# Kernel optimization log

Hardware: AMD Instinct MI355X
Metric: run time of the kernel (lower is better)

## Reference

```python
import jax, jax.numpy as jnp
import numpy as np

DIM = 2048
NUM_HEADS = 16
HEAD_DIM = DIM // NUM_HEADS  # 128
HIDDEN = HEAD_DIM * NUM_HEADS  # 2048


def setup_inputs() -> dict:
    key = jax.random.key(0)
    k1, k2, k3 = jax.random.split(key, 3)
    x = jax.random.normal(k1, (2, 4096, DIM), dtype=jnp.float32)
    # match torch init: gates.weight ~ N(0, dim**-0.5), output.weight ~ N(0, hidden**-0.5)
    Wg = jax.random.normal(k2, (NUM_HEADS + 3 * HIDDEN, DIM), dtype=jnp.float32) * DIM ** -0.5
    bg = jnp.zeros((NUM_HEADS + 3 * HIDDEN,), dtype=jnp.float32)
    Wo = jax.random.normal(k3, (DIM, HIDDEN), dtype=jnp.float32) * HIDDEN ** -0.5
    bo = jnp.zeros((DIM,), dtype=jnp.float32)
    return {"x": x, "Wg": Wg, "bg": bg, "Wo": Wo, "bo": bo}


def _combine(a, b):
    # linear recurrence c_t = f_t * c_{t-1} + u_t as an associative op
    fa, ua = a
    fb, ub = b
    return fa * fb, fb * ua + ub


def reference(x, Wg, bg, Wo, bo):
    # x: [B, T, dim]
    g = jnp.einsum('btd,gd->btg', x, Wg) + bg  # [B, T, H + 3*hidden]
    f = jax.nn.sigmoid(g[..., :NUM_HEADS])  # [B, T, H]
    i = jax.nn.sigmoid(g[..., NUM_HEADS:NUM_HEADS + HIDDEN])
    t = jnp.tanh(g[..., NUM_HEADS + HIDDEN:NUM_HEADS + 2 * HIDDEN])
    o = g[..., NUM_HEADS + 2 * HIDDEN:]
    f = jnp.repeat(f, HEAD_DIM, axis=-1)  # tied forget gate per head -> [B, T, hidden]
    update = i * t
    # scan over time axis (axis=1)
    _, c = jax.lax.associative_scan(_combine, (f, update), axis=1)
    h = o * jnp.tanh(c)
    return jnp.einsum('bth,dh->btd', h, Wo) + bo
```

## Files before the change

kernel.cpp:

```cpp
#include <hip/hip_runtime.h>
#include <hip/hip_bf16.h>

#define DIM 2048
#define NHEADS 16
#define HEAD_DIM 128
#define HIDDEN 2048
#define SEQ 4096
#define BATCH 2
#define BT (BATCH * SEQ)
#define NSEG 64
#define SEGLEN (SEQ / NSEG)
#define N_GATE (3 * HIDDEN)

typedef __bf16 bf16_t;
typedef __bf16 bf16x8 __attribute__((ext_vector_type(8)));
typedef __bf16 bf16x4_t __attribute__((ext_vector_type(4)));
typedef float f32x4 __attribute__((ext_vector_type(4)));

__device__ __forceinline__ void gload_lds16(const void* g, void* l) {
  __builtin_amdgcn_global_load_lds(
      (const __attribute__((address_space(1))) void*)g,
      (__attribute__((address_space(3))) void*)l, 16, 0, 0);
}

#define MEMFENCE asm volatile("" ::: "memory")
#define BAR do { MEMFENCE; __builtin_amdgcn_s_barrier(); MEMFENCE; } while (0)
#define LGKM0 do { asm volatile("s_waitcnt lgkmcnt(0)" ::: "memory"); \
                   __builtin_amdgcn_sched_barrier(0); } while (0)
#define VMCNT(n) asm volatile("s_waitcnt vmcnt(" #n ")" ::: "memory")

__global__ void cvt_f32_bf16(const float* __restrict__ src, bf16_t* __restrict__ dst, int n4) {
  int i = blockIdx.x * blockDim.x + threadIdx.x;
  if (i >= n4) return;
  float4 v = reinterpret_cast<const float4*>(src)[i];
  bf16x4_t o;
  o[0] = (bf16_t)v.x; o[1] = (bf16_t)v.y; o[2] = (bf16_t)v.z; o[3] = (bf16_t)v.w;
  reinterpret_cast<bf16x4_t*>(dst)[i] = o;
}

__global__ void fgate_kernel(const float* __restrict__ x, const float* __restrict__ Wg,
                             const float* __restrict__ bg, float* __restrict__ fout) {
  int idx = blockIdx.x * 256 + threadIdx.x;
  int bt = idx >> 4, h = idx & 15;
  const float* xr = x + (size_t)bt * DIM;
  const float* wr = Wg + (size_t)h * DIM;
  float acc = 0.f;
  for (int k = 0; k < DIM; k += 4) {
    float4 xv = *reinterpret_cast<const float4*>(xr + k);
    float4 wv = *reinterpret_cast<const float4*>(wr + k);
    acc = fmaf(xv.x, wv.x, acc);
    acc = fmaf(xv.y, wv.y, acc);
    acc = fmaf(xv.z, wv.z, acc);
    acc = fmaf(xv.w, wv.w, acc);
  }
  acc += bg[h];
  fout[idx] = 1.f / (1.f + expf(-acc));
}


__device__ __forceinline__ void stage_unit(const bf16_t* __restrict__ G, int grow0, int gcol,
                                           bf16_t* region, int rh, int wid, int lane) {
  const int r = rh * 128 + wid * 16 + (lane >> 2);
  const int c = (lane & 3) ^ ((lane >> 2) & 3);
  gload_lds16(G + (size_t)(grow0 + r) * 2048 + gcol + c * 8,
              region + (rh * 128 + wid * 16) * 32);
}

template <int MODE>
__global__ __launch_bounds__(512, 1)
void gemm256(const bf16_t* __restrict__ A, const bf16_t* __restrict__ B,
             const float* __restrict__ bias,
             bf16_t* __restrict__ Oi, bf16_t* __restrict__ Ot, bf16_t* __restrict__ Oo,
             float* __restrict__ Of, int tiles_n) {
  __shared__ __align__(16) bf16_t As[2][2][256 * 32];
  __shared__ __align__(16) bf16_t Bs[2][2][256 * 32];
  constexpr int KT = 32;

  const int tid = threadIdx.x;
  const int wid = tid >> 6, lane = tid & 63;
  const int nwg = gridDim.x, bid = blockIdx.x;
  const int swz = (bid & 7) * (nwg >> 3) + (bid >> 3);
  const int tm = swz / tiles_n, tn = swz - tm * tiles_n;
  const int brow = tm * 256, bcol = tn * 256;
  const int wm = wid >> 2, wn = wid & 3;
  const int rl = lane & 15, q = lane >> 4;
  const int fo = (q ^ (rl & 3)) << 3;
  const int arow0 = wm * 128 + rl;
  const int brow0 = wn * 64 + rl;

  f32x4 acc[8][4] = {};

#define FRAG(regptr, row) (*reinterpret_cast<const bf16x8*>(&(regptr)[(row) * 32 + fo]))

#pragma unroll
  for (int rh = 0; rh < 2; ++rh) stage_unit(A, brow, 0,      &As[0][0][0], rh, wid, lane);
#pragma unroll
  for (int rh = 0; rh < 2; ++rh) stage_unit(B, bcol, 0,      &Bs[0][0][0], rh, wid, lane);
#pragma unroll
  for (int rh = 0; rh < 2; ++rh) stage_unit(A, brow, 32,     &As[0][1][0], rh, wid, lane);
#pragma unroll
  for (int rh = 0; rh < 2; ++rh) stage_unit(B, bcol, 32,     &Bs[0][1][0], rh, wid, lane);
#pragma unroll
  for (int rh = 0; rh < 2; ++rh) stage_unit(A, brow, 64,     &As[1][0][0], rh, wid, lane);
#pragma unroll
  for (int rh = 0; rh < 2; ++rh) stage_unit(B, bcol, 64,     &Bs[1][0][0], rh, wid, lane);
  VMCNT(8);
  BAR;

  for (int t = 0; t < KT; ++t) {
    const int slot = t & 1, nslot = slot ^ 1;
    const bool s1 = (t + 1) < KT, s2 = (t + 2) < KT;
    const int kc1 = (t + 1) * 64, kc2 = (t + 2) * 64;
    const bf16_t* a0 = &As[slot][0][0];
    const bf16_t* a1 = &As[slot][1][0];
    const bf16_t* b0 = &Bs[slot][0][0];
    const bf16_t* b1 = &Bs[slot][1][0];
    bf16x8 bf[4], af[4];

#pragma unroll
    for (int ni = 0; ni < 4; ++ni) bf[ni] = FRAG(b0, brow0 + ni * 16);
#pragma unroll
    for (int mi = 0; mi < 4; ++mi) af[mi] = FRAG(a0, arow0 + mi * 16);
    if (s1) { stage_unit(A, brow, kc1 + 32, &As[nslot][1][0], 0, wid, lane);
              stage_unit(A, brow, kc1 + 32, &As[nslot][1][0], 1, wid, lane); }
    BAR; LGKM0;
    __builtin_amdgcn_s_setprio(1);
#pragma unroll
    for (int mi = 0; mi < 4; ++mi)
#pragma unroll
      for (int ni = 0; ni < 4; ++ni)
        acc[mi][ni] = __builtin_amdgcn_mfma_f32_16x16x32_bf16(af[mi], bf[ni], acc[mi][ni], 0, 0, 0);
    __builtin_amdgcn_s_setprio(0);
    BAR;

#pragma unroll
    for (int mi = 0; mi < 4; ++mi) af[mi] = FRAG(a0, arow0 + 64 + mi * 16);
    if (s1) { stage_unit(B, bcol, kc1 + 32, &Bs[nslot][1][0], 0, wid, lane);
              stage_unit(B, bcol, kc1 + 32, &Bs[nslot][1][0], 1, wid, lane); }
    BAR; LGKM0;
    __builtin_amdgcn_s_setprio(1);
#pragma unroll
    for (int mi = 0; mi < 4; ++mi)
#pragma unroll
      for (int ni = 0; ni < 4; ++ni)
        acc[4 + mi][ni] = __builtin_amdgcn_mfma_f32_16x16x32_bf16(af[mi], bf[ni], acc[4 + mi][ni], 0, 0, 0);
    __builtin_amdgcn_s_setprio(0);
    if (t < KT - 1) { VMCNT(8); } else { VMCNT(0); }
    BAR;

#pragma unroll
    for (int ni = 0; ni < 4; ++ni) bf[ni] = FRAG(b1, brow0 + ni * 16);
#pragma unroll
    for (int mi = 0; mi < 4; ++mi) af[mi] = FRAG(a1, arow0 + mi * 16);
    if (s2) { stage_unit(A, brow, kc2, &As[slot][0][0], 0, wid, lane);
              stage_unit(A, brow, kc2, &As[slot][0][0], 1, wid, lane); }
    BAR; LGKM0;
    __builtin_amdgcn_s_setprio(1);
#pragma unroll
    for (int mi = 0; mi < 4; ++mi)
#pragma unroll
      for (int ni = 0; ni < 4; ++ni)
        acc[mi][ni] = __builtin_amdgcn_mfma_f32_16x16x32_bf16(af[mi], bf[ni], acc[mi][ni], 0, 0, 0);
    __builtin_amdgcn_s_setprio(0);
    BAR;

#pragma unroll
    for (int mi = 0; mi < 4; ++mi) af[mi] = FRAG(a1, arow0 + 64 + mi * 16);
    if (s2) { stage_unit(B, bcol, kc2, &Bs[slot][0][0], 0, wid, lane);
              stage_unit(B, bcol, kc2, &Bs[slot][0][0], 1, wid, lane); }
    BAR; LGKM0;
    __builtin_amdgcn_s_setprio(1);
#pragma unroll
    for (int mi = 0; mi < 4; ++mi)
#pragma unroll
      for (int ni = 0; ni < 4; ++ni)
        acc[4 + mi][ni] = __builtin_amdgcn_mfma_f32_16x16x32_bf16(af[mi], bf[ni], acc[4 + mi][ni], 0, 0, 0);
    __builtin_amdgcn_s_setprio(0);
    if (t < KT - 2) { VMCNT(8); } else if (t == KT - 2) { VMCNT(4); } else { VMCNT(0); }
    BAR;
  }
#undef FRAG

  const int crow0 = brow + wm * 128;
  const int ccol0 = bcol + wn * 64;
  if (MODE == 0) {
    const int section = bcol >> 11;
    bf16_t* dst = (section == 0) ? Oi : ((section == 1) ? Ot : Oo);
#pragma unroll
    for (int mi = 0; mi < 8; ++mi)
#pragma unroll
      for (int ni = 0; ni < 4; ++ni) {
        int gcol = ccol0 + ni * 16 + (lane & 15);
        int col = gcol & 2047;
        float b = bias[gcol];
#pragma unroll
        for (int qq = 0; qq < 4; ++qq) {
          int row = crow0 + mi * 16 + (lane >> 4) * 4 + qq;
          float v = acc[mi][ni][qq] + b;
          float a;
          if (section == 0)      a = 1.f / (1.f + __expf(-v));
          else if (section == 1) a = tanhf(v);
          else                   a = v;
          dst[(size_t)row * HIDDEN + col] = (bf16_t)a;
        }
      }
  } else {
#pragma unroll
    for (int mi = 0; mi < 8; ++mi)
#pragma unroll
      for (int ni = 0; ni < 4; ++ni) {
        int col = ccol0 + ni * 16 + (lane & 15);
        float b = bias[col];
#pragma unroll
        for (int qq = 0; qq < 4; ++qq) {
          int row = crow0 + mi * 16 + (lane >> 4) * 4 + qq;
          Of[(size_t)row * DIM + col] = acc[mi][ni][qq] + b;
        }
      }
  }
}

__global__ void scan_pass1(const float* __restrict__ fg, const bf16_t* __restrict__ gi,
                           const bf16_t* __restrict__ gt, float* __restrict__ cend,
                           float* __restrict__ pseg) {
  int bx = blockIdx.x;
  int chblk = bx & 7, seg = (bx >> 3) & 63, b = bx >> 9;
  int ch = chblk * 256 + threadIdx.x;
  int head = ch >> 7;
  float c = 0.f, P = 1.f;
  size_t t0 = (size_t)b * SEQ + (size_t)seg * SEGLEN;
  for (int tt = 0; tt < SEGLEN; ++tt) {
    size_t bt = t0 + tt;
    float f = fg[bt * NHEADS + head];
    float iv = (float)gi[bt * HIDDEN + ch];
    float tv = (float)gt[bt * HIDDEN + ch];
    c = fmaf(f, c, iv * tv);
    P *= f;
  }
  size_t o = ((size_t)b * NSEG + seg) * HIDDEN + ch;
  cend[o] = c;
  pseg[o] = P;
}

__global__ void scan_pass2(const float* __restrict__ cend, const float* __restrict__ pseg,
                           float* __restrict__ cin) {
  int idx = blockIdx.x * 256 + threadIdx.x;
  int b = idx >> 11, ch = idx & 2047;
  float C = 0.f;
  for (int s = 0; s < NSEG; ++s) {
    size_t o = ((size_t)b * NSEG + s) * HIDDEN + ch;
    cin[o] = C;
    C = cend[o] + pseg[o] * C;
  }
}

__global__ void scan_pass3(const float* __restrict__ fg, const bf16_t* __restrict__ gi,
                           const bf16_t* __restrict__ gt, const bf16_t* __restrict__ go,
                           const float* __restrict__ cin, bf16_t* __restrict__ h) {
  int bx = blockIdx.x;
  int chblk = bx & 7, seg = (bx >> 3) & 63, b = bx >> 9;
  int ch = chblk * 256 + threadIdx.x;
  int head = ch >> 7;
  float c = cin[((size_t)b * NSEG + seg) * HIDDEN + ch];
  size_t t0 = (size_t)b * SEQ + (size_t)seg * SEGLEN;
  for (int tt = 0; tt < SEGLEN; ++tt) {
    size_t bt = t0 + tt;
    float f = fg[bt * NHEADS + head];
    float iv = (float)gi[bt * HIDDEN + ch];
    float tv = (float)gt[bt * HIDDEN + ch];
    c = fmaf(f, c, iv * tv);
    float hv = (float)go[bt * HIDDEN + ch] * tanhf(c);
    h[bt * HIDDEN + ch] = (bf16_t)hv;
  }
}

extern "C" void kernel_launch(void* const* d_in, const int* in_sizes, int n_in,
                              void* d_out, int out_size, void* d_ws, size_t ws_size,
                              hipStream_t stream) {
  const float* x  = (const float*)d_in[0];
  const float* Wg = (const float*)d_in[1];
  const float* bg = (const float*)d_in[2];
  const float* Wo = (const float*)d_in[3];
  const float* bo = (const float*)d_in[4];
  float* out = (float*)d_out;

  char* ws = (char*)d_ws;
  size_t off = 0;
  auto alloc = [&](size_t bytes) -> void* {
    void* p = ws + off;
    off += (bytes + 255) & ~(size_t)255;
    return p;
  };
  bf16_t* xb   = (bf16_t*)alloc((size_t)BT * DIM * 2);
  bf16_t* wgb  = (bf16_t*)alloc((size_t)N_GATE * DIM * 2);
  bf16_t* wob  = (bf16_t*)alloc((size_t)DIM * HIDDEN * 2);
  float*  fg   = (float*)alloc((size_t)BT * NHEADS * 4);
  bf16_t* gi   = (bf16_t*)alloc((size_t)BT * HIDDEN * 2);
  bf16_t* gt   = (bf16_t*)alloc((size_t)BT * HIDDEN * 2);
  bf16_t* go   = (bf16_t*)alloc((size_t)BT * HIDDEN * 2);
  bf16_t* hbuf = (bf16_t*)alloc((size_t)BT * HIDDEN * 2);
  float*  cend = (float*)alloc((size_t)BATCH * NSEG * HIDDEN * 4);
  float*  pseg = (float*)alloc((size_t)BATCH * NSEG * HIDDEN * 4);
  float*  cin  = (float*)alloc((size_t)BATCH * NSEG * HIDDEN * 4);
  (void)ws_size; (void)in_sizes; (void)n_in; (void)out_size;

  {
    int n4 = BT * DIM / 4;
    cvt_f32_bf16<<<(n4 + 255) / 256, 256, 0, stream>>>(x, xb, n4);
  }
  {
    int n4 = N_GATE * DIM / 4;
    cvt_f32_bf16<<<(n4 + 255) / 256, 256, 0, stream>>>(Wg + (size_t)NHEADS * DIM, wgb, n4);
  }
  {
    int n4 = DIM * HIDDEN / 4;
    cvt_f32_bf16<<<(n4 + 255) / 256, 256, 0, stream>>>(Wo, wob, n4);
  }

  fgate_kernel<<<(BT * NHEADS) / 256, 256, 0, stream>>>(x, Wg, bg, fg);

  gemm256<0><<<768, 512, 0, stream>>>(xb, wgb, bg + NHEADS, gi, gt, go, nullptr, 24);

  scan_pass1<<<BATCH * NSEG * (HIDDEN / 256), 256, 0, stream>>>(fg, gi, gt, cend, pseg);
  scan_pass2<<<BATCH * HIDDEN / 256, 256, 0, stream>>>(cend, pseg, cin);
  scan_pass3<<<BATCH * NSEG * (HIDDEN / 256), 256, 0, stream>>>(fg, gi, gt, go, cin, hbuf);

  gemm256<1><<<256, 512, 0, stream>>>(hbuf, wob, bo, nullptr, nullptr, nullptr, out, 8);
}
```

Before: 599.3 us.

## Restructure GEMM LDS staging to 128x64 half-tiles with finer-grained load pipelining

Changes the LDS tile layout from 256x32 K-halves to 128-row by 64-K half-tiles with an 8-way XOR swizzle. The main loop now stages each next-K tile in four pieces interleaved with the four MFMA phases, and replaces the paired barriers with a single wait-and-barrier per half iteration. The aim is fewer barriers and better overlap of global-to-LDS loads with MFMA work. The new vmcnt accounting is subtle, and a miscount could race or stall.

```diff
diff --git a/kernel.cpp b/kernel.cpp
--- a/kernel.cpp
+++ b/kernel.cpp
@@ -58,13 +58,15 @@
 }
 
 
-__device__ __forceinline__ void stage_unit(const bf16_t* __restrict__ G, int grow0, int gcol,
-                                           bf16_t* region, int rh, int wid, int lane) {
-  const int r = rh * 128 + wid * 16 + (lane >> 2);
-  const int c = (lane & 3) ^ ((lane >> 2) & 3);
-  gload_lds16(G + (size_t)(grow0 + r) * 2048 + gcol + c * 8,
-              region + (rh * 128 + wid * 16) * 32);
-}
+__device__ __forceinline__ void stage_unit(const bf16_t* __restrict__ G, int grow0, int kcol,
+                                           bf16_t* region, int j, int wid, int lane) {
+  const int r = j * 64 + wid * 8 + (lane >> 3);
+  const int c = (lane & 7) ^ (lane >> 3);
+  gload_lds16(G + (size_t)(grow0 + r) * 2048 + kcol + c * 8,
+              region + (size_t)(j * 64 + wid * 8) * 64);
+}
+
+#define FRAG8(ptr, row, fo) (*reinterpret_cast<const bf16x8*>(&(ptr)[(size_t)(row) * 64 + (fo)]))
 
 template <int MODE>
 __global__ __launch_bounds__(512, 1)
@@ -72,8 +74,8 @@
              const float* __restrict__ bias,
              bf16_t* __restrict__ Oi, bf16_t* __restrict__ Ot, bf16_t* __restrict__ Oo,
              float* __restrict__ Of, int tiles_n) {
-  __shared__ __align__(16) bf16_t As[2][2][256 * 32];
-  __shared__ __align__(16) bf16_t Bs[2][2][256 * 32];
+  __shared__ __align__(16) bf16_t As[2][2][128 * 64];
+  __shared__ __align__(16) bf16_t Bs[2][2][128 * 64];
   constexpr int KT = 32;
 
   const int tid = threadIdx.x;
@@ -84,102 +86,90 @@
   const int brow = tm * 256, bcol = tn * 256;
   const int wm = wid >> 2, wn = wid & 3;
   const int rl = lane & 15, q = lane >> 4;
-  const int fo = (q ^ (rl & 3)) << 3;
-  const int arow0 = wm * 128 + rl;
-  const int brow0 = wn * 64 + rl;
+  const int cx = rl & 7;
+  const int fo0 = ((q ^ cx) << 3);
+  const int fo1 = fo0 ^ 32;
+  const int bnh = wn >> 1, brl = (wn & 1) * 64;
 
   f32x4 acc[8][4] = {};
 
-#define FRAG(regptr, row) (*reinterpret_cast<const bf16x8*>(&(regptr)[(row) * 32 + fo]))
-
-#pragma unroll
-  for (int rh = 0; rh < 2; ++rh) stage_unit(A, brow, 0,      &As[0][0][0], rh, wid, lane);
-#pragma unroll
-  for (int rh = 0; rh < 2; ++rh) stage_unit(B, bcol, 0,      &Bs[0][0][0], rh, wid, lane);
-#pragma unroll
-  for (int rh = 0; rh < 2; ++rh) stage_unit(A, brow, 32,     &As[0][1][0], rh, wid, lane);
-#pragma unroll
-  for (int rh = 0; rh < 2; ++rh) stage_unit(B, bcol, 32,     &Bs[0][1][0], rh, wid, lane);
-#pragma unroll
-  for (int rh = 0; rh < 2; ++rh) stage_unit(A, brow, 64,     &As[1][0][0], rh, wid, lane);
-#pragma unroll
-  for (int rh = 0; rh < 2; ++rh) stage_unit(B, bcol, 64,     &Bs[1][0][0], rh, wid, lane);
-  VMCNT(8);
-  BAR;
+  stage_unit(B, bcol,       0, &Bs[0][0][0], 0, wid, lane);
+  stage_unit(B, bcol,       0, &Bs[0][0][0], 1, wid, lane);
+  stage_unit(B, bcol + 128, 0, &Bs[0][1][0], 0, wid, lane);
+  stage_unit(B, bcol + 128, 0, &Bs[0][1][0], 1, wid, lane);
+  stage_unit(A, brow,       0, &As[0][0][0], 0, wid, lane);
+  stage_unit(A, brow + 128, 0, &As[0][1][0], 0, wid, lane);
+  stage_unit(A, brow,       0, &As[0][0][0], 1, wid, lane);
+  stage_unit(A, brow + 128, 0, &As[0][1][0], 1, wid, lane);
 
   for (int t = 0; t < KT; ++t) {
-    const int slot = t & 1, nslot = slot ^ 1;
-    const bool s1 = (t + 1) < KT, s2 = (t + 2) < KT;
-    const int kc1 = (t + 1) * 64, kc2 = (t + 2) * 64;
-    const bf16_t* a0 = &As[slot][0][0];
-    const bf16_t* a1 = &As[slot][1][0];
-    const bf16_t* b0 = &Bs[slot][0][0];
-    const bf16_t* b1 = &Bs[slot][1][0];
-    bf16x8 bf[4], af[4];
-
-#pragma unroll
-    for (int ni = 0; ni < 4; ++ni) bf[ni] = FRAG(b0, brow0 + ni * 16);
-#pragma unroll
-    for (int mi = 0; mi < 4; ++mi) af[mi] = FRAG(a0, arow0 + mi * 16);
-    if (s1) { stage_unit(A, brow, kc1 + 32, &As[nslot][1][0], 0, wid, lane);
-              stage_unit(A, brow, kc1 + 32, &As[nslot][1][0], 1, wid, lane); }
-    BAR; LGKM0;
+    const int s = t & 1, ns = s ^ 1;
+    const bool s1 = (t + 1) < KT;
+    const int kc1 = (t + 1) * 64;
+    const bf16_t* a = &As[s][wm][0];
+    const bf16_t* b = &Bs[s][bnh][0];
+    bf16x8 af[4], bf[4];
+
+    VMCNT(2);
+    BAR;
+    if (s1) { stage_unit(B, bcol,       kc1, &Bs[ns][0][0], 0, wid, lane);
+              stage_unit(B, bcol,       kc1, &Bs[ns][0][0], 1, wid, lane); }
+#pragma unroll
+    for (int ni = 0; ni < 4; ++ni) bf[ni] = FRAG8(b, brl + ni * 16 + rl, fo0);
+#pragma unroll
+    for (int m = 0; m < 4; ++m)    af[m]  = FRAG8(a, m * 16 + rl, fo0);
+    LGKM0;
     __builtin_amdgcn_s_setprio(1);
 #pragma unroll
-    for (int mi = 0; mi < 4; ++mi)
+    for (int m = 0; m < 4; ++m)
 #pragma unroll
       for (int ni = 0; ni < 4; ++ni)
-        acc[mi][ni] = __builtin_amdgcn_mfma_f32_16x16x32_bf16(af[mi], bf[ni], acc[mi][ni], 0, 0, 0);
+        acc[m][ni] = __builtin_amdgcn_mfma_f32_16x16x32_bf16(af[m], bf[ni], acc[m][ni], 0, 0, 0);
     __builtin_amdgcn_s_setprio(0);
+
+    if (s1) { VMCNT(2); } else { VMCNT(0); }
     BAR;
-
-#pragma unroll
-    for (int mi = 0; mi < 4; ++mi) af[mi] = FRAG(a0, arow0 + 64 + mi * 16);
-    if (s1) { stage_unit(B, bcol, kc1 + 32, &Bs[nslot][1][0], 0, wid, lane);
-              stage_unit(B, bcol, kc1 + 32, &Bs[nslot][1][0], 1, wid, lane); }
-    BAR; LGKM0;
+    if (s1) { stage_unit(B, bcol + 128, kc1, &Bs[ns][1][0], 0, wid, lane);
+              stage_unit(B, bcol + 128, kc1, &Bs[ns][1][0], 1, wid, lane); }
+#pragma unroll
+    for (int m = 0; m < 4; ++m) af[m] = FRAG8(a, 64 + m * 16 + rl, fo0);
+    LGKM0;
     __builtin_amdgcn_s_setprio(1);
 #pragma unroll
-    for (int mi = 0; mi < 4; ++mi)
+    for (int m = 0; m < 4; ++m)
 #pragma unroll
       for (int ni = 0; ni < 4; ++ni)
-        acc[4 + mi][ni] = __builtin_amdgcn_mfma_f32_16x16x32_bf16(af[mi], bf[ni], acc[4 + mi][ni], 0, 0, 0);
+        acc[4 + m][ni] = __builtin_amdgcn_mfma_f32_16x16x32_bf16(af[m], bf[ni], acc[4 + m][ni], 0, 0, 0);
     __builtin_amdgcn_s_setprio(0);
-    if (t < KT - 1) { VMCNT(8); } else { VMCNT(0); }
-    BAR;
-
-#pragma unroll
-    for (int ni = 0; ni < 4; ++ni) bf[ni] = FRAG(b1, brow0 + ni * 16);
-#pragma unroll
-    for (int mi = 0; mi < 4; ++mi) af[mi] = FRAG(a1, arow0 + mi * 16);
-    if (s2) { stage_unit(A, brow, kc2, &As[slot][0][0], 0, wid, lane);
-              stage_unit(A, brow, kc2, &As[slot][0][0], 1, wid, lane); }
-    BAR; LGKM0;
+
+    if (s1) { stage_unit(A, brow,       kc1, &As[ns][0][0], 0, wid, lane);
+              stage_unit(A, brow + 128, kc1, &As[ns][1][0], 0, wid, lane); }
+#pragma unroll
+    for (int ni = 0; ni < 4; ++ni) bf[ni] = FRAG8(b, brl + ni * 16 + rl, fo1);
+#pragma unroll
+    for (int m = 0; m < 4; ++m)    af[m]  = FRAG8(a, m * 16 + rl, fo1);
+    LGKM0;
     __builtin_amdgcn_s_setprio(1);
 #pragma unroll
-    for (int mi = 0; mi < 4; ++mi)
+    for (int m = 0; m < 4; ++m)
 #pragma unroll
       for (int ni = 0; ni < 4; ++ni)
-        acc[mi][ni] = __builtin_amdgcn_mfma_f32_16x16x32_bf16(af[mi], bf[ni], acc[mi][ni], 0, 0, 0);
+        acc[m][ni] = __builtin_amdgcn_mfma_f32_16x16x32_bf16(af[m], bf[ni], acc[m][ni], 0, 0, 0);
     __builtin_amdgcn_s_setprio(0);
-    BAR;
-
-#pragma unroll
-    for (int mi = 0; mi < 4; ++mi) af[mi] = FRAG(a1, arow0 + 64 + mi * 16);
-    if (s2) { stage_unit(B, bcol, kc2, &Bs[slot][0][0], 0, wid, lane);
-              stage_unit(B, bcol, kc2, &Bs[slot][0][0], 1, wid, lane); }
-    BAR; LGKM0;
+
+    if (s1) { stage_unit(A, brow,       kc1, &As[ns][0][0], 1, wid, lane);
+              stage_unit(A, brow + 128, kc1, &As[ns][1][0], 1, wid, lane); }
+#pragma unroll
+    for (int m = 0; m < 4; ++m) af[m] = FRAG8(a, 64 + m * 16 + rl, fo1);
+    LGKM0;
     __builtin_amdgcn_s_setprio(1);
 #pragma unroll
-    for (int mi = 0; mi < 4; ++mi)
+    for (int m = 0; m < 4; ++m)
 #pragma unroll
       for (int ni = 0; ni < 4; ++ni)
-        acc[4 + mi][ni] = __builtin_amdgcn_mfma_f32_16x16x32_bf16(af[mi], bf[ni], acc[4 + mi][ni], 0, 0, 0);
+        acc[4 + m][ni] = __builtin_amdgcn_mfma_f32_16x16x32_bf16(af[m], bf[ni], acc[4 + m][ni], 0, 0, 0);
     __builtin_amdgcn_s_setprio(0);
-    if (t < KT - 2) { VMCNT(8); } else if (t == KT - 2) { VMCNT(4); } else { VMCNT(0); }
-    BAR;
-  }
-#undef FRAG
+  }
 
   const int crow0 = brow + wm * 128;
   const int ccol0 = bcol + wn * 64;
@@ -192,16 +182,16 @@
       for (int ni = 0; ni < 4; ++ni) {
         int gcol = ccol0 + ni * 16 + (lane & 15);
         int col = gcol & 2047;
-        float b = bias[gcol];
+        float bv = bias[gcol];
 #pragma unroll
         for (int qq = 0; qq < 4; ++qq) {
           int row = crow0 + mi * 16 + (lane >> 4) * 4 + qq;
-          float v = acc[mi][ni][qq] + b;
-          float a;
-          if (section == 0)      a = 1.f / (1.f + __expf(-v));
-          else if (section == 1) a = tanhf(v);
-          else                   a = v;
-          dst[(size_t)row * HIDDEN + col] = (bf16_t)a;
+          float v = acc[mi][ni][qq] + bv;
+          float aout;
+          if (section == 0)      aout = 1.f / (1.f + __expf(-v));
+          else if (section == 1) aout = tanhf(v);
+          else                   aout = v;
+          dst[(size_t)row * HIDDEN + col] = (bf16_t)aout;
         }
       }
   } else {
@@ -210,11 +200,11 @@
 #pragma unroll
       for (int ni = 0; ni < 4; ++ni) {
         int col = ccol0 + ni * 16 + (lane & 15);
-        float b = bias[col];
+        float bv = bias[col];
 #pragma unroll
         for (int qq = 0; qq < 4; ++qq) {
           int row = crow0 + mi * 16 + (lane >> 4) * 4 + qq;
-          Of[(size_t)row * DIM + col] = acc[mi][ni][qq] + b;
+          Of[(size_t)row * DIM + col] = acc[mi][ni][qq] + bv;
         }
       }
   }
```

Measured after the change: 610.2 us. No clear change (+1.8%).
